# Performance work log

Measured on AMD Instinct MI355X. Metric: run time of the kernel, lower is better.

## Reference

```python
import jax, jax.numpy as jnp
import numpy as np
from jax import lax

DN = ('NHWC', 'HWIO', 'NHWC')


def conv_same(x, w):
    return lax.conv_general_dilated(x, w, window_strides=(1, 1), padding='SAME',
                                    dimension_numbers=DN)


def dwconv(x, w):
    # w: (kh, kw, F, 1) TF depthwise layout -> HWIO (kh, kw, 1, F), groups=F
    F = w.shape[2]
    return lax.conv_general_dilated(x, jnp.transpose(w, (0, 1, 3, 2)),
                                    window_strides=(1, 1), padding='SAME',
                                    dimension_numbers=DN, feature_group_count=F)


def hard_sigmoid(x):
    return jnp.clip(0.2 * x + 0.5, 0.0, 1.0)


def setup_inputs() -> dict:
    key = jax.random.key(0)
    ks = jax.random.split(key, 10)
    B, H, W, Cin, F = 16, 128, 128, 64, 64
    s = 0.05
    return {
        'inputs': jax.random.normal(ks[0], (B, H, W, Cin), jnp.float32),
        'h0': jax.random.normal(ks[1], (B, H, W, F), jnp.float32),
        'c0': jax.random.normal(ks[2], (B, H, W, F), jnp.float32),
        'm0': jax.random.normal(ks[3], (B, H, W, F), jnp.float32),
        'kernel': jax.random.normal(ks[4], (3, 3, Cin, 4 * F), jnp.float32) * s,
        'recurrent_kernel': jax.random.normal(ks[5], (3, 3, F, 4 * F), jnp.float32) * s,
        'bias': jnp.concatenate([jnp.zeros((F,), jnp.float32),
                                 jnp.ones((F,), jnp.float32),
                                 jnp.zeros((2 * F,), jnp.float32)]),
        'sa_kernel': jax.random.normal(ks[6], (1, 1, F, 5), jnp.float32) * s,
        'kernel_z': jax.random.normal(ks[7], (3, 3, 2, F), jnp.float32) * s,
        'depth_wise_kernel': jax.random.normal(ks[8], (3, 3, F, 6), jnp.float32) * s,
        'sa_bias': jnp.zeros((3 * F,), jnp.float32),
    }


def reference(inputs, h0, c0, m0, kernel, recurrent_kernel, bias, sa_kernel,
              kernel_z, depth_wise_kernel, sa_bias):
    F = h0.shape[-1]
    # --- ConvLSTM gates (no dropout: all four gates share the same input, so
    # a single fused conv over the 4F-channel kernel is the same math) ---
    xz = conv_same(inputs, kernel) + bias  # [B,H,W,4F]
    hz = conv_same(h0, recurrent_kernel)   # [B,H,W,4F]
    z = xz + hz
    zi_, zf_, zc_, zo_ = jnp.split(z, 4, axis=-1)
    i = hard_sigmoid(zi_)
    f = hard_sigmoid(zf_)
    c = f * c0 + i * jnp.tanh(zc_)
    o = hard_sigmoid(zo_)
    h = o * jnp.tanh(c)  # [B,H,W,F]

    # --- Self-attention memory (SAM) module; 1x1 convs -> channel contractions ---
    w = sa_kernel[0, 0]  # [F,5]
    v_h = jnp.einsum('bhwc,c->bhw', h, w[:, 0])
    k_h = jnp.einsum('bhwc,c->bhw', h, w[:, 1])
    q_h = jnp.einsum('bhwc,c->bhw', h, w[:, 2])
    k_m = jnp.einsum('bhwc,c->bhw', m0, w[:, 3])
    v_m = jnp.einsum('bhwc,c->bhw', m0, w[:, 4])

    alpha_m = jax.nn.softmax(jnp.matmul(q_h, k_m), axis=-1)  # [B,H,H] (H==W)
    alpha_h = jax.nn.softmax(jnp.matmul(q_h, k_h), axis=-1)
    z_m = jnp.matmul(alpha_m, v_m)  # [B,H,W]
    z_h = jnp.matmul(alpha_h, v_h)

    zi = conv_same(jnp.stack([z_h, z_m], axis=-1), kernel_z)  # [B,H,W,F]

    dw = depth_wise_kernel  # [3,3,F,6]
    b_i, b_g, b_o = jnp.split(sa_bias, 3)
    i2 = jax.nn.sigmoid(dwconv(zi, dw[..., 0:1]) + dwconv(h, dw[..., 1:2]) + b_i)
    g = jnp.tanh(dwconv(zi, dw[..., 2:3]) + dwconv(h, dw[..., 3:4]) + b_g)
    o2 = jax.nn.sigmoid(dwconv(zi, dw[..., 4:5]) + dwconv(h, dw[..., 5:6]) + b_o)

    m_t = (1.0 - i2) * m0 + i2 * g
    h_hat = m_t * o2
    return h_hat, c, m_t
```

## Files before the change

kernel.cpp:

```cpp
#include <hip/hip_runtime.h>

#define BB 16
#define HH 128
#define WW 128
#define FF 64
#define NPIX (BB*HH*WW)

typedef short bf16x8 __attribute__((ext_vector_type(8)));
typedef float f32x4 __attribute__((ext_vector_type(4)));

__device__ __forceinline__ float bf2f(unsigned int u){ return __uint_as_float(u<<16); }
__device__ __forceinline__ unsigned short f2bf(float f){
  unsigned u = __float_as_uint(f);
  u += 0x7fffu + ((u>>16)&1u);
  return (unsigned short)(u>>16);
}
__device__ __forceinline__ float hsig(float x){ return fminf(fmaxf(fmaf(0.2f,x,0.5f),0.f),1.f); }
__device__ __forceinline__ float tanh_fast(float x){
  float e = __expf(2.f*x);
  return 1.f - 2.f/(e + 1.f);
}
__device__ __forceinline__ void gload_lds16(const void* g, void* l){
  __builtin_amdgcn_global_load_lds(
      (const __attribute__((address_space(1))) unsigned int*)g,
      (__attribute__((address_space(3))) unsigned int*)l, 16, 0, 0);
}

__global__ __launch_bounds__(256) void zero_pads(unsigned short* __restrict__ Xp){
  int i = blockIdx.x*256 + threadIdx.x;
  if (i >= 16*516) return;
  int b = i / 516, r = i % 516;
  int y, x;
  if (r < 130){ y = 0; x = r; }
  else if (r < 260){ y = 129; x = r-130; }
  else if (r < 388){ y = r-260+1; x = 0; }
  else { y = r-388+1; x = 129; }
  unsigned short* p = Xp + (((size_t)(b*130 + y)*130) + x)*128;
  uint4 z = {0u,0u,0u,0u};
  #pragma unroll
  for (int c=0;c<16;++c) ((uint4*)p)[c] = z;
}

__global__ __launch_bounds__(256) void prep_x(const float* __restrict__ in,
                                              const float* __restrict__ h0,
                                              unsigned short* __restrict__ Xp){
  int gi = blockIdx.x*256 + threadIdx.x;
  int pix = gi >> 4;
  int ch8 = (gi & 15) * 8;
  const float* src = (ch8 < 64) ? (in + (size_t)pix*64 + ch8)
                                : (h0 + (size_t)pix*64 + (ch8-64));
  float4 v0 = *(const float4*)src;
  float4 v1 = *(const float4*)(src+4);
  uint4 o;
  o.x = (unsigned)f2bf(v0.x) | ((unsigned)f2bf(v0.y)<<16);
  o.y = (unsigned)f2bf(v0.z) | ((unsigned)f2bf(v0.w)<<16);
  o.z = (unsigned)f2bf(v1.x) | ((unsigned)f2bf(v1.y)<<16);
  o.w = (unsigned)f2bf(v1.z) | ((unsigned)f2bf(v1.w)<<16);
  int b = pix >> 14, y = (pix >> 7) & 127, x = pix & 127;
  *(uint4*)(Xp + (((size_t)(b*130 + y+1)*130) + (x+1))*128 + ch8) = o;
}

__global__ __launch_bounds__(256) void prep_w(const float* __restrict__ kern,
                                              const float* __restrict__ rkern,
                                              unsigned short* __restrict__ Wg){
  int k = blockIdx.x;
  int n = threadIdx.x;
  int tap = k >> 7, c = k & 127;
  float v = (c < 64) ? kern[((size_t)(tap*64 + c))*256 + n]
                     : rkern[((size_t)(tap*64 + (c-64)))*256 + n];
  Wg[(size_t)n*1152 + k] = f2bf(v);
}

__global__ __launch_bounds__(256, 2) void gates_kernel(
    const unsigned short* __restrict__ Xp,
    const unsigned short* __restrict__ Wg,
    const float* __restrict__ bias,
    const float* __restrict__ c0,
    float* __restrict__ c_out,
    unsigned short* __restrict__ h_bf){
  __shared__ unsigned short As[130*128];
  const int gid = blockIdx.x;
  const int swz = (gid & 7)*256 + (gid >> 3);
  const int b  = swz >> 7;
  const int y  = swz & 127;
  const int tid = threadIdx.x;
  const int l = tid & 63;
  const int wid = tid >> 6;
  const int l15 = l & 15, l4 = l >> 4;
  const int n0 = wid*16 + l15;

  const unsigned short* brow[4];
  #pragma unroll
  for (int g=0; g<4; ++g) brow[g] = Wg + (size_t)(g*64 + n0)*1152 + l4*8;

  f32x4 acc[8][4];
  #pragma unroll
  for (int mf=0;mf<8;++mf)
    #pragma unroll
    for (int g=0;g<4;++g) acc[mf][g] = (f32x4){0.f,0.f,0.f,0.f};

  auto stage = [&](int dyi){
    const unsigned short* gbase = Xp + ((size_t)((b*130 + y + dyi)*130))*128;
    unsigned short* lbase = &As[0];
    #pragma unroll
    for (int it=0; it<8; ++it){
      int q = it*256 + tid;
      int px = q >> 4, c = q & 15;
      int cs = c ^ (px & 7);
      gload_lds16(gbase + (size_t)px*128 + cs*8, lbase + (size_t)q*8);
    }
    if (tid < 32){
      int q = 2048 + tid;
      int px = q >> 4, c = q & 15;
      int cs = c ^ (px & 7);
      gload_lds16(gbase + (size_t)px*128 + cs*8, lbase + (size_t)q*8);
    }
  };

  for (int dyi = 0; dyi < 3; ++dyi){
    stage(dyi);
    __syncthreads();
    const unsigned short* asb = &As[0];
    #pragma unroll
    for (int dxi = 0; dxi < 3; ++dxi){
      const int tap = dyi*3 + dxi;
      #pragma unroll
      for (int ksc = 0; ksc < 2; ++ksc){
        bf16x8 bfr[4][2];
        #pragma unroll
        for (int g=0; g<4; ++g)
          #pragma unroll
          for (int k2=0; k2<2; ++k2)
            bfr[g][k2] = *(const bf16x8*)(brow[g] + tap*128 + (ksc*2+k2)*32);
        #pragma unroll
        for (int k2=0; k2<2; ++k2){
          const int cd = (ksc*2+k2)*4 + l4;
          #pragma unroll
          for (int mf=0; mf<8; ++mf){
            const int px = mf*16 + l15 + dxi;
            bf16x8 a = *(const bf16x8*)(asb + (size_t)px*128 + ((cd ^ (px & 7))*8));
            #pragma unroll
            for (int g=0;g<4;++g)
              acc[mf][g] = __builtin_amdgcn_mfma_f32_16x16x32_bf16(a, bfr[g][k2], acc[mf][g], 0,0,0);
          }
        }
      }
    }
    __syncthreads();
  }
  const float b0 = bias[n0], b1 = bias[64+n0], b2 = bias[128+n0], b3 = bias[192+n0];
  const size_t prow = (size_t)(b*128 + y)*128;
  #pragma unroll
  for (int mf=0;mf<8;++mf){
    #pragma unroll
    for (int r=0;r<4;++r){
      const int x = mf*16 + l4*4 + r;
      const size_t p = prow + x;
      const float zi_ = acc[mf][0][r] + b0;
      const float zf_ = acc[mf][1][r] + b1;
      const float zc_ = acc[mf][2][r] + b2;
      const float zo_ = acc[mf][3][r] + b3;
      const float iv = hsig(zi_), fv = hsig(zf_), ov = hsig(zo_);
      const float cv = fv*c0[p*64 + n0] + iv*tanh_fast(zc_);
      const float hv = ov*tanh_fast(cv);
      c_out[p*64 + n0] = cv;
      h_bf[p*64 + n0] = f2bf(hv);
    }
  }
}

__global__ __launch_bounds__(256) void qkv_kernel(
    const unsigned short* __restrict__ h_bf, const float* __restrict__ m0,
    const float* __restrict__ sak,
    float* __restrict__ q_h, float* __restrict__ k_h, float* __restrict__ v_h,
    float* __restrict__ k_m, float* __restrict__ v_m){
  __shared__ float wS[320];
  for (int i = threadIdx.x; i < 320; i += 256) wS[i] = sak[i];
  __syncthreads();
  const int p = blockIdx.x*256 + threadIdx.x;
  const unsigned short* hp = h_bf + (size_t)p*64;
  const float* mp = m0 + (size_t)p*64;
  float a0=0,a1=0,a2=0,a3=0,a4=0;
  #pragma unroll
  for (int ch = 0; ch < 64; ch += 8){
    uint4 hu = *(const uint4*)(hp + ch);
    float4 ma = *(const float4*)(mp + ch);
    float4 mb = *(const float4*)(mp + ch + 4);
    float hv[8] = { bf2f(hu.x&0xffffu), bf2f(hu.x>>16), bf2f(hu.y&0xffffu), bf2f(hu.y>>16),
                    bf2f(hu.z&0xffffu), bf2f(hu.z>>16), bf2f(hu.w&0xffffu), bf2f(hu.w>>16) };
    float mv[8] = { ma.x,ma.y,ma.z,ma.w, mb.x,mb.y,mb.z,mb.w };
    #pragma unroll
    for (int jj=0;jj<8;++jj){
      const float* w = &wS[(ch+jj)*5];
      a0 = fmaf(hv[jj], w[0], a0);
      a1 = fmaf(hv[jj], w[1], a1);
      a2 = fmaf(hv[jj], w[2], a2);
      a3 = fmaf(mv[jj], w[3], a3);
      a4 = fmaf(mv[jj], w[4], a4);
    }
  }
  v_h[p]=a0; k_h[p]=a1; q_h[p]=a2; k_m[p]=a3; v_m[p]=a4;
}

__global__ __launch_bounds__(256) void attn_kernel(
    const float* __restrict__ q_h, const float* __restrict__ k_h, const float* __restrict__ v_h,
    const float* __restrict__ k_m, const float* __restrict__ v_m,
    float* __restrict__ z_h, float* __restrict__ z_m){
  __shared__ float q2[2][128];
  __shared__ float al[2][128];
  __shared__ float redm[2][2], reds[2][2];
  const int bid = blockIdx.x;
  const int b = bid >> 5;
  const int type = (bid >> 4) & 1;
  const int rb = bid & 15;
  const float* K = (type ? k_m : k_h) + (size_t)b*16384;
  const float* V = (type ? v_m : v_h) + (size_t)b*16384;
  const float* Q = q_h + (size_t)b*16384;
  float* Z = (type ? z_m : z_h) + (size_t)b*16384;
  const int t = threadIdx.x, rg = t>>7, j = t&127, lane = t&63, hw = (t>>6)&1;
  for (int it = 0; it < 4; ++it){
    const int i = rb*8 + it*2 + rg;
    __syncthreads();
    q2[rg][j] = Q[i*128 + j];
    __syncthreads();
    float s = 0.f;
    #pragma unroll 8
    for (int w=0; w<128; ++w) s = fmaf(q2[rg][w], K[w*128 + j], s);
    float mx = s;
    #pragma unroll
    for (int o=1;o<64;o<<=1) mx = fmaxf(mx, __shfl_xor(mx, o));
    if (lane==0) redm[rg][hw] = mx;
    __syncthreads();
    mx = fmaxf(redm[rg][0], redm[rg][1]);
    float pe = __expf(s - mx);
    float sm = pe;
    #pragma unroll
    for (int o=1;o<64;o<<=1) sm += __shfl_xor(sm, o);
    if (lane==0) reds[rg][hw] = sm;
    __syncthreads();
    const float inv = 1.f/(reds[rg][0]+reds[rg][1]);
    al[rg][j] = pe*inv;
    __syncthreads();
    float z = 0.f;
    #pragma unroll 8
    for (int w=0; w<128; ++w) z = fmaf(al[rg][w], V[w*128 + j], z);
    Z[i*128 + j] = z;
  }
}

__global__ __launch_bounds__(512) void zconv_kernel(
    const float* __restrict__ z_h, const float* __restrict__ z_m,
    const float* __restrict__ kz, unsigned short* __restrict__ zi_bf){
  const int f = threadIdx.x & 63;
  const int g = threadIdx.x >> 6;
  const int row = blockIdx.x;
  const int y = row & 127;
  float w0[9], w1[9];
  #pragma unroll
  for (int tap=0; tap<9; ++tap){
    w0[tap] = kz[tap*128 + f];
    w1[tap] = kz[tap*128 + 64 + f];
  }
  const float* zhr = z_h + (size_t)row*128;
  const float* zmr = z_m + (size_t)row*128;
  const bool ym = (y > 0), yp = (y < 127);
  float az[3][3], am[3][3];
  auto ldc = [&](int x, float (&Z)[3], float (&M)[3]){
    if ((unsigned)x < 128u){
      Z[0] = ym ? zhr[x-128] : 0.f;  M[0] = ym ? zmr[x-128] : 0.f;
      Z[1] = zhr[x];                 M[1] = zmr[x];
      Z[2] = yp ? zhr[x+128] : 0.f;  M[2] = yp ? zmr[x+128] : 0.f;
    } else { Z[0]=Z[1]=Z[2]=0.f; M[0]=M[1]=M[2]=0.f; }
  };
  const int x0 = g*16;
  ldc(x0-1, az[0], am[0]);
  ldc(x0,   az[1], am[1]);
  for (int i=0; i<16; ++i){
    const int x = x0 + i;
    ldc(x+1, az[2], am[2]);
    float acc = 0.f;
    #pragma unroll
    for (int tap=0; tap<9; ++tap){
      const int dy = tap/3, dx = tap%3;
      acc = fmaf(az[dx][dy], w0[tap], acc);
      acc = fmaf(am[dx][dy], w1[tap], acc);
    }
    zi_bf[((size_t)row*128 + x)*64 + f] = f2bf(acc);
    #pragma unroll
    for (int k=0;k<3;++k){
      az[0][k]=az[1][k]; az[1][k]=az[2][k];
      am[0][k]=am[1][k]; am[1][k]=am[2][k];
    }
  }
}

__global__ __launch_bounds__(256) void final_kernel(
    const unsigned short* __restrict__ zi_bf, const unsigned short* __restrict__ h_bf,
    const float* __restrict__ m0, const float* __restrict__ dwk,
    const float* __restrict__ sab,
    float* __restrict__ hhat, float* __restrict__ m_t){
  const int f = threadIdx.x & 63;
  const int g = threadIdx.x >> 6;
  const int row = blockIdx.x;
  const int y = row & 127;
  float wv[9][6];
  #pragma unroll
  for (int tap=0;tap<9;++tap)
    #pragma unroll
    for (int jj=0;jj<6;++jj) wv[tap][jj] = dwk[(tap*64 + f)*6 + jj];
  const float bi = sab[f], bg = sab[64+f], bo = sab[128+f];
  const bool ym = (y > 0), yp = (y < 127);
  const size_t rb = (size_t)row*128;
  float vz[3][3], vh[3][3];
  auto ldc = [&](int x, float (&Z)[3], float (&H)[3]){
    if ((unsigned)x < 128u){
      const size_t base = (rb + x)*64 + f;
      Z[0] = ym ? bf2f(zi_bf[base - 8192]) : 0.f;
      H[0] = ym ? bf2f(h_bf [base - 8192]) : 0.f;
      Z[1] = bf2f(zi_bf[base]);
      H[1] = bf2f(h_bf [base]);
      Z[2] = yp ? bf2f(zi_bf[base + 8192]) : 0.f;
      H[2] = yp ? bf2f(h_bf [base + 8192]) : 0.f;
    } else { Z[0]=Z[1]=Z[2]=0.f; H[0]=H[1]=H[2]=0.f; }
  };
  const int x0 = g*32;
  ldc(x0-1, vz[0], vh[0]);
  ldc(x0,   vz[1], vh[1]);
  for (int i=0; i<32; ++i){
    const int x = x0 + i;
    ldc(x+1, vz[2], vh[2]);
    float si=0.f, sg=0.f, so=0.f;
    #pragma unroll
    for (int tap=0;tap<9;++tap){
      const int dy = tap/3, dx = tap%3;
      const float zv = vz[dx][dy], hv = vh[dx][dy];
      si = fmaf(zv, wv[tap][0], si); si = fmaf(hv, wv[tap][1], si);
      sg = fmaf(zv, wv[tap][2], sg); sg = fmaf(hv, wv[tap][3], sg);
      so = fmaf(zv, wv[tap][4], so); so = fmaf(hv, wv[tap][5], so);
    }
    const size_t p = rb + x;
    const float i2 = 1.f/(1.f+__expf(-(si+bi)));
    const float gg = tanh_fast(sg+bg);
    const float o2 = 1.f/(1.f+__expf(-(so+bo)));
    const float mv = m0[p*64+f];
    const float mt = (1.f-i2)*mv + i2*gg;
    hhat[p*64+f] = mt*o2;
    m_t[p*64+f]  = mt;
    #pragma unroll
    for (int k=0;k<3;++k){
      vz[0][k]=vz[1][k]; vz[1][k]=vz[2][k];
      vh[0][k]=vh[1][k]; vh[1][k]=vh[2][k];
    }
  }
}

extern "C" void kernel_launch(void* const* d_in, const int* in_sizes, int n_in,
                              void* d_out, int out_size, void* d_ws, size_t ws_size,
                              hipStream_t stream){
  const float* inputs = (const float*)d_in[0];
  const float* h0p    = (const float*)d_in[1];
  const float* c0p    = (const float*)d_in[2];
  const float* m0p    = (const float*)d_in[3];
  const float* kern   = (const float*)d_in[4];
  const float* rkern  = (const float*)d_in[5];
  const float* biasp  = (const float*)d_in[6];
  const float* sakp   = (const float*)d_in[7];
  const float* kzp    = (const float*)d_in[8];
  const float* dwkp   = (const float*)d_in[9];
  const float* sabp   = (const float*)d_in[10];
  float* out = (float*)d_out;
  char* ws = (char*)d_ws;

  constexpr size_t SZ_XP  = (size_t)16*130*130*128*2;
  constexpr size_t SZ_WG  = (size_t)256*1152*2;
  constexpr size_t SZ_HBF = (size_t)NPIX*64*2;
  constexpr size_t SZA    = (size_t)NPIX*4;
  constexpr size_t OFF_XP  = 0;
  constexpr size_t OFF_WG  = OFF_XP + SZ_XP;
  constexpr size_t OFF_HBF = OFF_WG + SZ_WG;
  constexpr size_t OFF_Q   = OFF_HBF + SZ_HBF;
  constexpr size_t OFF_KH  = OFF_Q  + SZA;
  constexpr size_t OFF_VH  = OFF_KH + SZA;
  constexpr size_t OFF_KM  = OFF_VH + SZA;
  constexpr size_t OFF_VM  = OFF_KM + SZA;
  constexpr size_t OFF_ZH  = OFF_VM + SZA;
  constexpr size_t OFF_ZM  = OFF_ZH + SZA;
  constexpr size_t OFF_ZI  = OFF_ZM + SZA;

  unsigned short* Xp  = (unsigned short*)(ws + OFF_XP);
  unsigned short* Wg  = (unsigned short*)(ws + OFF_WG);
  unsigned short* Hbf = (unsigned short*)(ws + OFF_HBF);
  float* Qh = (float*)(ws + OFF_Q);
  float* Kh = (float*)(ws + OFF_KH);
  float* Vh = (float*)(ws + OFF_VH);
  float* Km = (float*)(ws + OFF_KM);
  float* Vm = (float*)(ws + OFF_VM);
  float* Zh = (float*)(ws + OFF_ZH);
  float* Zm = (float*)(ws + OFF_ZM);
  unsigned short* ZIbf = (unsigned short*)(ws + OFF_ZI);

  zero_pads<<<33, 256, 0, stream>>>(Xp);
  prep_x<<<NPIX*16/256, 256, 0, stream>>>(inputs, h0p, Xp);
  prep_w<<<1152, 256, 0, stream>>>(kern, rkern, Wg);
  gates_kernel<<<2048, 256, 0, stream>>>(Xp, Wg, biasp, c0p,
                                         out + (size_t)NPIX*64, Hbf);
  qkv_kernel<<<NPIX/256, 256, 0, stream>>>(Hbf, m0p, sakp, Qh, Kh, Vh, Km, Vm);
  attn_kernel<<<512, 256, 0, stream>>>(Qh, Kh, Vh, Km, Vm, Zh, Zm);
  zconv_kernel<<<2048, 512, 0, stream>>>(Zh, Zm, kzp, ZIbf);
  final_kernel<<<2048, 256, 0, stream>>>(ZIbf, Hbf, m0p, dwkp, sabp,
                                         out, out + 2*(size_t)NPIX*64);
}
```

Baseline: 421.9 us.

## Split gates conv tiles to half-rows and double-buffer LDS with B-fragment prefetch

The gates GEMM-conv kernel now processes half a row (64 pixels) per block instead of a full row, doubling the grid and halving accumulator registers. The LDS input strip is double-buffered so the next dy strip loads asynchronously while MFMAs run on the current one. Weight fragments are software-pipelined in two register slots, and s_setprio wraps the MFMA phases. This aims to hide global-load and sync latency and raise occupancy. The cost is weights re-read by twice as many blocks and a 2-pixel halo reloaded per half-row.

Result: slower. 518.4 us (+22.9%).

```diff
diff --git a/kernel.cpp b/kernel.cpp
--- a/kernel.cpp
+++ b/kernel.cpp
@@ -78,11 +78,12 @@
     const float* __restrict__ c0,
     float* __restrict__ c_out,
     unsigned short* __restrict__ h_bf){
-  __shared__ unsigned short As[130*128];
+  __shared__ unsigned short As[2][66*128];
   const int gid = blockIdx.x;
-  const int swz = (gid & 7)*256 + (gid >> 3);
-  const int b  = swz >> 7;
-  const int y  = swz & 127;
+  const int swz = (gid & 7)*512 + (gid >> 3);
+  const int b  = swz >> 8;
+  const int y  = (swz >> 1) & 127;
+  const int xh = swz & 1;
   const int tid = threadIdx.x;
   const int l = tid & 63;
   const int wid = tid >> 6;
@@ -93,65 +94,82 @@
   #pragma unroll
   for (int g=0; g<4; ++g) brow[g] = Wg + (size_t)(g*64 + n0)*1152 + l4*8;
 
-  f32x4 acc[8][4];
-  #pragma unroll
-  for (int mf=0;mf<8;++mf)
+  f32x4 acc[4][4];
+  #pragma unroll
+  for (int mf=0;mf<4;++mf)
     #pragma unroll
     for (int g=0;g<4;++g) acc[mf][g] = (f32x4){0.f,0.f,0.f,0.f};
 
-  auto stage = [&](int dyi){
-    const unsigned short* gbase = Xp + ((size_t)((b*130 + y + dyi)*130))*128;
-    unsigned short* lbase = &As[0];
-    #pragma unroll
-    for (int it=0; it<8; ++it){
+  auto stage = [&](int buf, int dyi){
+    const unsigned short* gbase =
+        Xp + ((size_t)((b*130 + y + dyi)*130) + xh*64)*128;
+    unsigned short* lbase = &As[buf][0];
+    #pragma unroll
+    for (int it=0; it<4; ++it){
       int q = it*256 + tid;
       int px = q >> 4, c = q & 15;
       int cs = c ^ (px & 7);
       gload_lds16(gbase + (size_t)px*128 + cs*8, lbase + (size_t)q*8);
     }
     if (tid < 32){
-      int q = 2048 + tid;
+      int q = 1024 + tid;
       int px = q >> 4, c = q & 15;
       int cs = c ^ (px & 7);
       gload_lds16(gbase + (size_t)px*128 + cs*8, lbase + (size_t)q*8);
     }
   };
 
-  for (int dyi = 0; dyi < 3; ++dyi){
-    stage(dyi);
-    __syncthreads();
-    const unsigned short* asb = &As[0];
-    #pragma unroll
-    for (int dxi = 0; dxi < 3; ++dxi){
-      const int tap = dyi*3 + dxi;
+  auto runStrip = [&](int dyi){
+    const unsigned short* asb = &As[dyi & 1][0];
+    bf16x8 bfr[2][4][2];
+    auto loadB = [&](int slot, int kp){
+      const int tap = dyi*3 + (kp >> 1), ksc = kp & 1;
       #pragma unroll
-      for (int ksc = 0; ksc < 2; ++ksc){
-        bf16x8 bfr[4][2];
+      for (int g=0; g<4; ++g)
         #pragma unroll
-        for (int g=0; g<4; ++g)
+        for (int k2=0; k2<2; ++k2)
+          bfr[slot][g][k2] = *(const bf16x8*)(brow[g] + tap*128 + (ksc*2 + k2)*32);
+    };
+    auto mfmaPhase = [&](int slot, int kp){
+      const int dxi = kp >> 1, ksc = kp & 1;
+      __builtin_amdgcn_s_setprio(1);
+      #pragma unroll
+      for (int k2=0; k2<2; ++k2){
+        const int cd = (ksc*2 + k2)*4 + l4;
+        #pragma unroll
+        for (int mf=0; mf<4; ++mf){
+          const int px = mf*16 + l15 + dxi;
+          bf16x8 a = *(const bf16x8*)(asb + (size_t)px*128 + ((cd ^ (px & 7))*8));
           #pragma unroll
-          for (int k2=0; k2<2; ++k2)
-            bfr[g][k2] = *(const bf16x8*)(brow[g] + tap*128 + (ksc*2+k2)*32);
-        #pragma unroll
-        for (int k2=0; k2<2; ++k2){
-          const int cd = (ksc*2+k2)*4 + l4;
-          #pragma unroll
-          for (int mf=0; mf<8; ++mf){
-            const int px = mf*16 + l15 + dxi;
-            bf16x8 a = *(const bf16x8*)(asb + (size_t)px*128 + ((cd ^ (px & 7))*8));
-            #pragma unroll
-            for (int g=0;g<4;++g)
-              acc[mf][g] = __builtin_amdgcn_mfma_f32_16x16x32_bf16(a, bfr[g][k2], acc[mf][g], 0,0,0);
-          }
+          for (int g=0;g<4;++g)
+            acc[mf][g] = __builtin_amdgcn_mfma_f32_16x16x32_bf16(a, bfr[slot][g][k2], acc[mf][g], 0,0,0);
         }
       }
-    }
-    __syncthreads();
-  }
+      __builtin_amdgcn_s_setprio(0);
+    };
+    loadB(0,0); loadB(1,1);
+    mfmaPhase(0,0);
+    loadB(0,2);
+    if (dyi < 2) stage((dyi+1)&1, dyi+1);
+    mfmaPhase(1,1);
+    loadB(1,3);
+    mfmaPhase(0,2);
+    loadB(0,4);
+    mfmaPhase(1,3);
+    loadB(1,5);
+    mfmaPhase(0,4);
+    mfmaPhase(1,5);
+    __syncthreads();
+  };
+
+  stage(0,0);
+  __syncthreads();
+  runStrip(0); runStrip(1); runStrip(2);
+
   const float b0 = bias[n0], b1 = bias[64+n0], b2 = bias[128+n0], b3 = bias[192+n0];
-  const size_t prow = (size_t)(b*128 + y)*128;
-  #pragma unroll
-  for (int mf=0;mf<8;++mf){
+  const size_t prow = (size_t)(b*128 + y)*128 + xh*64;
+  #pragma unroll
+  for (int mf=0;mf<4;++mf){
     #pragma unroll
     for (int r=0;r<4;++r){
       const int x = mf*16 + l4*4 + r;
@@ -402,7 +420,7 @@
   zero_pads<<<33, 256, 0, stream>>>(Xp);
   prep_x<<<NPIX*16/256, 256, 0, stream>>>(inputs, h0p, Xp);
   prep_w<<<1152, 256, 0, stream>>>(kern, rkern, Wg);
-  gates_kernel<<<2048, 256, 0, stream>>>(Xp, Wg, biasp, c0p,
+  gates_kernel<<<4096, 256, 0, stream>>>(Xp, Wg, biasp, c0p,
                                          out + (size_t)NPIX*64, Hbf);
   qkv_kernel<<<NPIX/256, 256, 0, stream>>>(Hbf, m0p, sakp, Qh, Kh, Vh, Km, Vm);
   attn_kernel<<<512, 256, 0, stream>>>(Qh, Kh, Vh, Km, Vm, Zh, Zm);
```
